# Performance work log

Hardware: AMD Instinct MI355X
Metric: run time of the kernel (lower is better)

## Reference

```python
import jax, jax.numpy as jnp
import numpy as np
from jax import lax

EPS = 1e-5
DN = ('NCHW', 'OIHW', 'NCHW')


def setup_inputs() -> dict:
    key = jax.random.key(0)
    ks = jax.random.split(key, 16)
    B = 8192
    # uniform(0,1): every pixel nonzero => all voxels active => sparse conv == dense conv
    x = jax.random.uniform(ks[0], (B, 1, 28, 28), dtype=jnp.float32)

    def conv_params(kw, kb, c_in, c_out, k):
        scale = 1.0 / np.sqrt(c_in * k * k)
        w = jax.random.normal(kw, (c_out, c_in, k, k), dtype=jnp.float32) * scale
        b = jax.random.normal(kb, (c_out,), dtype=jnp.float32) * scale
        return w, b

    w0, b0 = conv_params(ks[1], ks[2], 1, 32, 3)
    w1, b1 = conv_params(ks[3], ks[4], 32, 64, 2)
    w2, b2 = conv_params(ks[5], ks[6], 64, 128, 2)
    # BatchNorm affine params (init: gamma=1, beta=0)
    g0, be0 = jnp.ones((32,), jnp.float32), jnp.zeros((32,), jnp.float32)
    g1, be1 = jnp.ones((64,), jnp.float32), jnp.zeros((64,), jnp.float32)
    g2, be2 = jnp.ones((128,), jnp.float32), jnp.zeros((128,), jnp.float32)
    w_fc = jax.random.normal(ks[7], (10, 128), dtype=jnp.float32) * (1.0 / np.sqrt(128))
    b_fc = jax.random.normal(ks[8], (10,), dtype=jnp.float32) * (1.0 / np.sqrt(128))
    return dict(x=x, w0=w0, b0=b0, g0=g0, be0=be0,
                w1=w1, b1=b1, g1=g1, be1=be1,
                w2=w2, b2=b2, g2=g2, be2=be2,
                w_fc=w_fc, b_fc=b_fc)


def _conv_bn_relu(x, w, b, g, be, stride, padding):
    # sparse conv on fully-active grid == dense conv
    y = lax.conv_general_dilated(x, w, (stride, stride), padding,
                                 dimension_numbers=DN)
    y = y + b[None, :, None, None]
    # BatchNorm1d over (N_active, C) == stats over batch+spatial (biased var)
    mean = jnp.mean(y, axis=(0, 2, 3))
    var = jnp.var(y, axis=(0, 2, 3))
    y = (y - mean[None, :, None, None]) * lax.rsqrt(var + EPS)[None, :, None, None]
    y = y * g[None, :, None, None] + be[None, :, None, None]
    return jax.nn.relu(y)


def reference(x, w0, b0, g0, be0, w1, b1, g1, be1, w2, b2, g2, be2, w_fc, b_fc):
    h = _conv_bn_relu(x, w0, b0, g0, be0, 1, 'SAME')    # (B,32,28,28)
    h = _conv_bn_relu(h, w1, b1, g1, be1, 2, 'VALID')   # (B,64,14,14)
    h = _conv_bn_relu(h, w2, b2, g2, be2, 2, 'VALID')   # (B,128,7,7)
    pooled = jnp.mean(h, axis=(2, 3))                    # AdaptiveAvgPool2d(1)+Flatten
    return pooled @ w_fc.T + b_fc                        # (B, n_classes)
```

## Files before the change

### kernel.cpp

```cpp
#include <hip/hip_runtime.h>
#include <hip/hip_bf16.h>

typedef __bf16 bf16x8 __attribute__((ext_vector_type(8)));
typedef float  f32x4  __attribute__((ext_vector_type(4)));

#define BSZ 8192

__global__ void k_prep(const float* __restrict__ w1, const float* __restrict__ w2,
                       __bf16* __restrict__ w1b, __bf16* __restrict__ w2b) {
    int t = blockIdx.x * blockDim.x + threadIdx.x;
    if (t < 8192) {
        int oc = t >> 7, k = t & 127, c = k & 31, d = k >> 5;
        w1b[t] = (__bf16)w1[oc * 128 + c * 4 + d];
    }
    if (t < 32768) {
        int oc = t >> 8, k = t & 255, c = k & 63, d = k >> 6;
        w2b[t] = (__bf16)w2[oc * 256 + c * 4 + d];
    }
}

__global__ __launch_bounds__(256) void k_stats0(const float* __restrict__ x,
                                                float* __restrict__ part0) {
    __shared__ float sred[4 * 54];
    const int tid = threadIdx.x;
    float a[54];
#pragma unroll
    for (int i = 0; i < 54; i++) a[i] = 0.f;
    const int total = BSZ * 784;
    for (int p = blockIdx.x * 256 + tid; p < total; p += gridDim.x * 256) {
        int b = p / 784, pix = p - b * 784;
        int y = pix / 28, xx = pix - y * 28;
        const float* xb = x + (long)b * 784;
        float nv[9];
#pragma unroll
        for (int dy = 0; dy < 3; dy++) {
            int yy = y + dy - 1;
#pragma unroll
            for (int dx = 0; dx < 3; dx++) {
                int x2 = xx + dx - 1;
                nv[dy * 3 + dx] = (yy >= 0 && yy < 28 && x2 >= 0 && x2 < 28) ? xb[yy * 28 + x2] : 0.f;
            }
        }
        int idx = 0;
#pragma unroll
        for (int t = 0; t < 9; t++) {
            float vt = nv[t];
            a[45 + t] += vt;
#pragma unroll
            for (int u = t; u < 9; u++) { a[idx] += vt * nv[u]; idx++; }
        }
    }
#pragma unroll
    for (int i = 0; i < 54; i++) {
        float v = a[i];
        v += __shfl_xor(v, 1);  v += __shfl_xor(v, 2);  v += __shfl_xor(v, 4);
        v += __shfl_xor(v, 8);  v += __shfl_xor(v, 16); v += __shfl_xor(v, 32);
        a[i] = v;
    }
    const int l = tid & 63, w = tid >> 6;
    if (l == 0) {
#pragma unroll
        for (int i = 0; i < 54; i++) sred[w * 54 + i] = a[i];
    }
    __syncthreads();
    if (tid < 54)
        part0[blockIdx.x * 64 + tid] = sred[tid] + sred[54 + tid] + sred[108 + tid] + sred[162 + tid];
}

__global__ void k_fin0(const float* __restrict__ part0, const float* __restrict__ w0,
                       const float* __restrict__ g0, const float* __restrict__ be0,
                       float* __restrict__ abc0) {
    __shared__ float red[4 * 54];
    int t = threadIdx.x, c = t & 63, g = t >> 6;
    if (c < 54) {
        float acc = 0.f;
        for (int i = g; i < 1024; i += 4) acc += part0[i * 64 + c];
        red[g * 54 + c] = acc;
    }
    __syncthreads();
    if (t < 54) red[t] = red[t] + red[54 + t] + red[108 + t] + red[162 + t];
    __syncthreads();
    if (t < 32) {
        float wv[9];
#pragma unroll
        for (int tap = 0; tap < 9; tap++) wv[tap] = w0[t * 9 + tap];
        float sum = 0.f, sq = 0.f;
        int idx = 0;
#pragma unroll
        for (int ta = 0; ta < 9; ta++) {
            sum = fmaf(wv[ta], red[45 + ta], sum);
#pragma unroll
            for (int u = ta; u < 9; u++) {
                float coef = (u == ta) ? 1.f : 2.f;
                sq = fmaf(coef * wv[ta] * wv[u], red[idx], sq);
                idx++;
            }
        }
        float cnt = (float)BSZ * 784.f;
        float mean = sum / cnt;
        float var = sq / cnt - mean * mean;
        float A = g0[t] * rsqrtf(var + 1e-5f);
#pragma unroll
        for (int tap = 0; tap < 9; tap++)
            abc0[(t >> 3) * 72 + tap * 8 + (t & 7)] = A * wv[tap];
        abc0[288 + t] = be0[t] - mean * A;
    }
}

__global__ __launch_bounds__(256) void k_conv01(const float* __restrict__ x,
                                                const float* __restrict__ abc0,
                                                const __bf16* __restrict__ w1b,
                                                __bf16* __restrict__ h1,
                                                float* __restrict__ part1) {
    __shared__ float xs[30 * 30];
    __shared__ __attribute__((aligned(16))) __bf16 sAt[2][16 * 136];
    const int b = blockIdx.x, tid = threadIdx.x;
    if (tid < 116) {
        int idx;
        if (tid < 30)      idx = tid;
        else if (tid < 60) idx = 29 * 30 + (tid - 30);
        else if (tid < 88) idx = (tid - 60 + 1) * 30;
        else               idx = (tid - 88 + 1) * 30 + 29;
        xs[idx] = 0.f;
    }
    for (int j = tid; j < 784; j += 256) {
        int yy = j / 28, xx2 = j - yy * 28;
        xs[(yy + 1) * 30 + xx2 + 1] = x[(long)b * 784 + j];
    }
    const int pgu = __builtin_amdgcn_readfirstlane(tid >> 6);
    const float* wfp = abc0 + pgu * 72;
    float wf[72];
#pragma unroll
    for (int i = 0; i < 72; i++) wf[i] = wfp[i];
    float c0r[8];
#pragma unroll
    for (int j = 0; j < 8; j++) c0r[j] = abc0[288 + pgu * 8 + j];

    const int pi = tid & 15, pd = (tid >> 4) & 3;
    const int w = tid >> 6, l = tid & 63, q = l >> 4, n = l & 15;
    const int oc = w * 16 + n;
    bf16x8 fbv[4];
#pragma unroll
    for (int kc = 0; kc < 4; kc++)
        fbv[kc] = *(const bf16x8*)&w1b[oc * 128 + kc * 32 + q * 8];
    float ssum = 0.f, ssq = 0.f;
    __bf16* hb = h1 + (long)b * 12544 + (q * 4) * 64 + oc;
    __syncthreads();

    for (int mt = 0; mt < 13; mt++) {
        __bf16* dst = &sAt[mt & 1][pi * 136 + pd * 32 + pgu * 8];
        int m = mt * 16 + pi;
        bf16x8 pk;
        if (m < 196) {
            int my = m / 14, mx = m - my * 14;
            int y0 = my * 2 + (pd >> 1), x0 = mx * 2 + (pd & 1);
            float nv[9];
#pragma unroll
            for (int dy = 0; dy < 3; dy++)
#pragma unroll
                for (int dx = 0; dx < 3; dx++)
                    nv[dy * 3 + dx] = xs[(y0 + dy) * 30 + x0 + dx];
            float a[8];
#pragma unroll
            for (int j = 0; j < 8; j++) a[j] = c0r[j];
#pragma unroll
            for (int t = 0; t < 9; t++) {
                float nvt = nv[t];
#pragma unroll
                for (int j = 0; j < 8; j++) a[j] = fmaf(nvt, wf[t * 8 + j], a[j]);
            }
#pragma unroll
            for (int j = 0; j < 8; j++) pk[j] = (__bf16)fmaxf(a[j], 0.f);
        } else {
#pragma unroll
            for (int j = 0; j < 8; j++) pk[j] = (__bf16)0.0f;
        }
        *(bf16x8*)dst = pk;
        __syncthreads();
        const __bf16* sa = &sAt[mt & 1][n * 136 + q * 8];
        f32x4 acc = {0.f, 0.f, 0.f, 0.f};
#pragma unroll
        for (int kc = 0; kc < 4; kc++) {
            bf16x8 fav = *(const bf16x8*)&sa[kc * 32];
            acc = __builtin_amdgcn_mfma_f32_16x16x32_bf16(fav, fbv[kc], acc, 0, 0, 0);
        }
        bool valid = (mt < 12) | (q == 0);
        __bf16* hp = hb + mt * 16 * 64;
#pragma unroll
        for (int r = 0; r < 4; r++) {
            __bf16 hv = (__bf16)acc[r];
            if (valid) hp[r * 64] = hv;
            float fv = (float)hv;
            ssum += fv; ssq += fv * fv;
        }
    }
    ssum += __shfl_xor(ssum, 16); ssum += __shfl_xor(ssum, 32);
    ssq  += __shfl_xor(ssq, 16);  ssq  += __shfl_xor(ssq, 32);
    if (l < 16) {
        part1[(long)oc * BSZ + b] = ssum;
        part1[(long)(64 + oc) * BSZ + b] = ssq;
    }
}

__global__ __launch_bounds__(256) void k_redfin(const float* __restrict__ part,
                                                const float* __restrict__ g,
                                                const float* __restrict__ be,
                                                float* __restrict__ abc,
                                                int C, float cnt) {
    __shared__ float s1[256], s2[256];
    const int c = blockIdx.x, tid = threadIdx.x;
    float a = 0.f, bq = 0.f;
    const float* p1 = part + (long)c * BSZ;
    const float* p2 = part + (long)(C + c) * BSZ;
    for (int i = tid; i < BSZ; i += 256) { a += p1[i]; bq += p2[i]; }
    s1[tid] = a; s2[tid] = bq;
    __syncthreads();
    for (int s = 128; s > 0; s >>= 1) {
        if (tid < s) { s1[tid] += s1[tid + s]; s2[tid] += s2[tid + s]; }
        __syncthreads();
    }
    if (tid == 0) {
        float mean = s1[0] / cnt;
        float var = s2[0] / cnt - mean * mean;
        float A = g[c] * rsqrtf(var + 1e-5f);
        abc[c] = A;
        abc[C + c] = be[c] - mean * A;
    }
}

__global__ __launch_bounds__(256) void k_conv2s(__bf16* __restrict__ h1,
                                                const __bf16* __restrict__ w2b,
                                                const float* __restrict__ abc1,
                                                float* __restrict__ part2) {
    __shared__ __attribute__((aligned(16))) __bf16 sAt[2][16 * 264];
    __shared__ float sbn1[128];
    const int b = blockIdx.x, tid = threadIdx.x;
    if (tid < 128) sbn1[tid] = abc1[tid];
    const __bf16* src = h1 + (long)b * 12544;
    const int w = tid >> 6, l = tid & 63, q = l >> 4, n = l & 15;
    bf16x8 fbv[2][8];
#pragma unroll
    for (int ntl = 0; ntl < 2; ntl++) {
        int oc = (2 * w + ntl) * 16 + n;
#pragma unroll
        for (int kc = 0; kc < 8; kc++)
            fbv[ntl][kc] = *(const bf16x8*)&w2b[oc * 256 + kc * 32 + q * 8];
    }
    float ssum[2] = {0.f, 0.f}, ssq[2] = {0.f, 0.f};
    __bf16* zb = h1 + (long)b * 12544 + (q * 4) * 128 + (2 * w) * 16 + n;
    __syncthreads();

    for (int mt = 0; mt < 4; mt++) {
#pragma unroll
        for (int it = 0; it < 2; it++) {
            int idx = it * 256 + tid;
            int rl = idx >> 5, o = (idx & 31) * 8;
            int r = mt * 16 + rl;
            bf16x8 wv;
            if (r < 49) {
                int d = o >> 6, c = o & 63;
                int py = r / 7, px = r - py * 7;
                int msrc = (2 * py + (d >> 1)) * 14 + 2 * px + (d & 1);
                bf16x8 v = *(const bf16x8*)&src[msrc * 64 + c];
#pragma unroll
                for (int j = 0; j < 8; j++) {
                    float f = fmaxf((float)v[j] * sbn1[c + j] + sbn1[64 + c + j], 0.f);
                    wv[j] = (__bf16)f;
                }
            } else {
#pragma unroll
                for (int j = 0; j < 8; j++) wv[j] = (__bf16)0.0f;
            }
            *(bf16x8*)&sAt[mt & 1][rl * 264 + o] = wv;
        }
        __syncthreads();
        bf16x8 fav[8];
#pragma unroll
        for (int kc = 0; kc < 8; kc++)
            fav[kc] = *(const bf16x8*)&sAt[mt & 1][n * 264 + kc * 32 + q * 8];
#pragma unroll
        for (int ntl = 0; ntl < 2; ntl++) {
            f32x4 acc = {0.f, 0.f, 0.f, 0.f};
#pragma unroll
            for (int kc = 0; kc < 8; kc++)
                acc = __builtin_amdgcn_mfma_f32_16x16x32_bf16(fav[kc], fbv[ntl][kc], acc, 0, 0, 0);
            __bf16* zp = zb + mt * 16 * 128 + ntl * 16;
#pragma unroll
            for (int rr = 0; rr < 4; rr++) {
                __bf16 hv = (__bf16)acc[rr];
                int m = mt * 16 + q * 4 + rr;
                if (m < 49) zp[rr * 128] = hv;
                float fv = (float)hv;
                ssum[ntl] += fv; ssq[ntl] += fv * fv;
            }
        }
    }
#pragma unroll
    for (int ntl = 0; ntl < 2; ntl++) {
        ssum[ntl] += __shfl_xor(ssum[ntl], 16); ssum[ntl] += __shfl_xor(ssum[ntl], 32);
        ssq[ntl]  += __shfl_xor(ssq[ntl], 16);  ssq[ntl]  += __shfl_xor(ssq[ntl], 32);
    }
    if (l < 16) {
#pragma unroll
        for (int ntl = 0; ntl < 2; ntl++) {
            int oc = (2 * w + ntl) * 16 + l;
            part2[(long)oc * BSZ + b] = ssum[ntl];
            part2[(long)(128 + oc) * BSZ + b] = ssq[ntl];
        }
    }
}

__global__ __launch_bounds__(256) void k_final(const __bf16* __restrict__ z2,
                                               const float* __restrict__ abc2,
                                               const float* __restrict__ wfc,
                                               const float* __restrict__ bfc,
                                               float* __restrict__ out) {
    __shared__ float sbn2[256];
    __shared__ float pp[16 * 128];
    __shared__ float pooled[128];
    __shared__ float fcred[80];
    const int b = blockIdx.x, tid = threadIdx.x;
    sbn2[tid] = abc2[tid];
    __syncthreads();
    const int g = tid & 15, c0 = g * 8, rg = tid >> 4;
    const __bf16* src = z2 + (long)b * 12544;
    float acc[8];
#pragma unroll
    for (int q = 0; q < 8; q++) acc[q] = 0.f;
    for (int rr = rg; rr < 49; rr += 16) {
        bf16x8 v = *(const bf16x8*)&src[rr * 128 + c0];
#pragma unroll
        for (int q = 0; q < 8; q++) {
            float f = fmaxf((float)v[q] * sbn2[c0 + q] + sbn2[128 + c0 + q], 0.f);
            acc[q] += f;
        }
    }
    *(f32x4*)&pp[rg * 128 + c0]     = *(f32x4*)&acc[0];
    *(f32x4*)&pp[rg * 128 + c0 + 4] = *(f32x4*)&acc[4];
    __syncthreads();
    if (tid < 128) {
        float s = 0.f;
#pragma unroll
        for (int r = 0; r < 16; r++) s += pp[r * 128 + tid];
        pooled[tid] = s * (1.f / 49.f);
    }
    __syncthreads();
    if (tid < 80) {
        int o = tid >> 3, s = tid & 7;
        float a = 0.f;
#pragma unroll
        for (int j = 0; j < 16; j++) a = fmaf(pooled[s * 16 + j], wfc[o * 128 + s * 16 + j], a);
        fcred[tid] = a;
    }
    __syncthreads();
    if (tid < 10) {
        float a = bfc[tid];
#pragma unroll
        for (int s = 0; s < 8; s++) a += fcred[tid * 8 + s];
        out[(long)b * 10 + tid] = a;
    }
}

extern "C" void kernel_launch(void* const* d_in, const int* in_sizes, int n_in,
                              void* d_out, int out_size, void* d_ws, size_t ws_size,
                              hipStream_t stream) {
    const float* x   = (const float*)d_in[0];
    const float* w0  = (const float*)d_in[1];
    const float* g0  = (const float*)d_in[3];
    const float* be0 = (const float*)d_in[4];
    const float* w1  = (const float*)d_in[5];
    const float* g1  = (const float*)d_in[7];
    const float* be1 = (const float*)d_in[8];
    const float* w2  = (const float*)d_in[9];
    const float* g2  = (const float*)d_in[11];
    const float* be2 = (const float*)d_in[12];
    const float* wfc = (const float*)d_in[13];
    const float* bfc = (const float*)d_in[14];
    float* out = (float*)d_out;

    float* ws    = (float*)d_ws;
    float* part0 = ws;
    float* abc0  = part0 + 1024 * 64;
    float* part1 = abc0 + 320;
    float* abc1  = part1 + 128 * BSZ;
    float* part2 = abc1 + 128;
    float* abc2  = part2 + 256 * BSZ;
    __bf16* w1b  = (__bf16*)(abc2 + 256);
    __bf16* w2b  = w1b + 8192;
    __bf16* h1   = w2b + 32768;

    k_prep<<<dim3(128), dim3(256), 0, stream>>>(w1, w2, w1b, w2b);
    k_stats0<<<dim3(1024), dim3(256), 0, stream>>>(x, part0);
    k_fin0<<<dim3(1), dim3(256), 0, stream>>>(part0, w0, g0, be0, abc0);
    k_conv01<<<dim3(BSZ), dim3(256), 0, stream>>>(x, abc0, w1b, h1, part1);
    k_redfin<<<dim3(64), dim3(256), 0, stream>>>(part1, g1, be1, abc1, 64, (float)(BSZ * 196));
    k_conv2s<<<dim3(BSZ), dim3(256), 0, stream>>>(h1, w2b, abc1, part2);
    k_redfin<<<dim3(128), dim3(256), 0, stream>>>(part2, g2, be2, abc2, 128, (float)(BSZ * 49));
    k_final<<<dim3(BSZ), dim3(256), 0, stream>>>(h1, abc2, wfc, bfc, out);
}
```

Before: 431.2 us.

## Process four images per block and fold weight prep into stats kernel

The conv01, conv2s and final kernels now loop over four images per block, with grids a quarter the size. Per-block setup such as loading weight fragments, BN coefficients and the zeroed halo is paid once per four images instead of once per image. The weight bf16 conversion moves into k_stats0, which removes one kernel launch. conv2s now stages its output tile in shared memory so global stores are row-contiguous, at the cost of an extra barrier per tile. With fewer blocks there is less parallelism to hide latency, and each block has a longer serial chain.

```diff
diff --git a/kernel.cpp b/kernel.cpp
--- a/kernel.cpp
+++ b/kernel.cpp
@@ -6,23 +6,25 @@
 
 #define BSZ 8192
 
-__global__ void k_prep(const float* __restrict__ w1, const float* __restrict__ w2,
-                       __bf16* __restrict__ w1b, __bf16* __restrict__ w2b) {
-    int t = blockIdx.x * blockDim.x + threadIdx.x;
-    if (t < 8192) {
-        int oc = t >> 7, k = t & 127, c = k & 31, d = k >> 5;
-        w1b[t] = (__bf16)w1[oc * 128 + c * 4 + d];
-    }
-    if (t < 32768) {
-        int oc = t >> 8, k = t & 255, c = k & 63, d = k >> 6;
-        w2b[t] = (__bf16)w2[oc * 256 + c * 4 + d];
-    }
-}
-
 __global__ __launch_bounds__(256) void k_stats0(const float* __restrict__ x,
-                                                float* __restrict__ part0) {
+                                                float* __restrict__ part0,
+                                                const float* __restrict__ w1,
+                                                const float* __restrict__ w2,
+                                                __bf16* __restrict__ w1b,
+                                                __bf16* __restrict__ w2b) {
     __shared__ float sred[4 * 54];
     const int tid = threadIdx.x;
+    {
+        int t = blockIdx.x * 256 + tid;
+        if (t < 8192) {
+            int oc = t >> 7, k = t & 127, c = k & 31, d = k >> 5;
+            w1b[t] = (__bf16)w1[oc * 128 + c * 4 + d];
+        }
+        if (t < 32768) {
+            int oc = t >> 8, k = t & 255, c = k & 63, d = k >> 6;
+            w2b[t] = (__bf16)w2[oc * 256 + c * 4 + d];
+        }
+    }
     float a[54];
 #pragma unroll
     for (int i = 0; i < 54; i++) a[i] = 0.f;
@@ -43,11 +45,11 @@
         }
         int idx = 0;
 #pragma unroll
-        for (int t = 0; t < 9; t++) {
-            float vt = nv[t];
-            a[45 + t] += vt;
-#pragma unroll
-            for (int u = t; u < 9; u++) { a[idx] += vt * nv[u]; idx++; }
+        for (int t2 = 0; t2 < 9; t2++) {
+            float vt = nv[t2];
+            a[45 + t2] += vt;
+#pragma unroll
+            for (int u = t2; u < 9; u++) { a[idx] += vt * nv[u]; idx++; }
         }
     }
 #pragma unroll
@@ -114,7 +116,7 @@
                                                 float* __restrict__ part1) {
     __shared__ float xs[30 * 30];
     __shared__ __attribute__((aligned(16))) __bf16 sAt[2][16 * 136];
-    const int b = blockIdx.x, tid = threadIdx.x;
+    const int tid = threadIdx.x;
     if (tid < 116) {
         int idx;
         if (tid < 30)      idx = tid;
@@ -123,10 +125,6 @@
         else               idx = (tid - 88 + 1) * 30 + 29;
         xs[idx] = 0.f;
     }
-    for (int j = tid; j < 784; j += 256) {
-        int yy = j / 28, xx2 = j - yy * 28;
-        xs[(yy + 1) * 30 + xx2 + 1] = x[(long)b * 784 + j];
-    }
     const int pgu = __builtin_amdgcn_readfirstlane(tid >> 6);
     const float* wfp = abc0 + pgu * 72;
     float wf[72];
@@ -143,62 +141,69 @@
 #pragma unroll
     for (int kc = 0; kc < 4; kc++)
         fbv[kc] = *(const bf16x8*)&w1b[oc * 128 + kc * 32 + q * 8];
-    float ssum = 0.f, ssq = 0.f;
-    __bf16* hb = h1 + (long)b * 12544 + (q * 4) * 64 + oc;
-    __syncthreads();
-
-    for (int mt = 0; mt < 13; mt++) {
-        __bf16* dst = &sAt[mt & 1][pi * 136 + pd * 32 + pgu * 8];
-        int m = mt * 16 + pi;
-        bf16x8 pk;
-        if (m < 196) {
-            int my = m / 14, mx = m - my * 14;
-            int y0 = my * 2 + (pd >> 1), x0 = mx * 2 + (pd & 1);
-            float nv[9];
-#pragma unroll
-            for (int dy = 0; dy < 3; dy++)
-#pragma unroll
-                for (int dx = 0; dx < 3; dx++)
-                    nv[dy * 3 + dx] = xs[(y0 + dy) * 30 + x0 + dx];
-            float a[8];
-#pragma unroll
-            for (int j = 0; j < 8; j++) a[j] = c0r[j];
-#pragma unroll
-            for (int t = 0; t < 9; t++) {
-                float nvt = nv[t];
-#pragma unroll
-                for (int j = 0; j < 8; j++) a[j] = fmaf(nvt, wf[t * 8 + j], a[j]);
-            }
-#pragma unroll
-            for (int j = 0; j < 8; j++) pk[j] = (__bf16)fmaxf(a[j], 0.f);
-        } else {
-#pragma unroll
-            for (int j = 0; j < 8; j++) pk[j] = (__bf16)0.0f;
-        }
-        *(bf16x8*)dst = pk;
+
+    for (int img = 0; img < 4; img++) {
+        const int b = blockIdx.x * 4 + img;
+        for (int j = tid; j < 784; j += 256) {
+            int yy = j / 28, xx2 = j - yy * 28;
+            xs[(yy + 1) * 30 + xx2 + 1] = x[(long)b * 784 + j];
+        }
         __syncthreads();
-        const __bf16* sa = &sAt[mt & 1][n * 136 + q * 8];
-        f32x4 acc = {0.f, 0.f, 0.f, 0.f};
-#pragma unroll
-        for (int kc = 0; kc < 4; kc++) {
-            bf16x8 fav = *(const bf16x8*)&sa[kc * 32];
-            acc = __builtin_amdgcn_mfma_f32_16x16x32_bf16(fav, fbv[kc], acc, 0, 0, 0);
-        }
-        bool valid = (mt < 12) | (q == 0);
-        __bf16* hp = hb + mt * 16 * 64;
-#pragma unroll
-        for (int r = 0; r < 4; r++) {
-            __bf16 hv = (__bf16)acc[r];
-            if (valid) hp[r * 64] = hv;
-            float fv = (float)hv;
-            ssum += fv; ssq += fv * fv;
-        }
-    }
-    ssum += __shfl_xor(ssum, 16); ssum += __shfl_xor(ssum, 32);
-    ssq  += __shfl_xor(ssq, 16);  ssq  += __shfl_xor(ssq, 32);
-    if (l < 16) {
-        part1[(long)oc * BSZ + b] = ssum;
-        part1[(long)(64 + oc) * BSZ + b] = ssq;
+        float ssum = 0.f, ssq = 0.f;
+        __bf16* hb = h1 + (long)b * 12544 + (q * 4) * 64 + oc;
+        for (int mt = 0; mt < 13; mt++) {
+            __bf16* dst = &sAt[mt & 1][pi * 136 + pd * 32 + pgu * 8];
+            int m = mt * 16 + pi;
+            bf16x8 pk;
+            if (m < 196) {
+                int my = m / 14, mx = m - my * 14;
+                int y0 = my * 2 + (pd >> 1), x0 = mx * 2 + (pd & 1);
+                float nv[9];
+#pragma unroll
+                for (int dy = 0; dy < 3; dy++)
+#pragma unroll
+                    for (int dx = 0; dx < 3; dx++)
+                        nv[dy * 3 + dx] = xs[(y0 + dy) * 30 + x0 + dx];
+                float a[8];
+#pragma unroll
+                for (int j = 0; j < 8; j++) a[j] = c0r[j];
+#pragma unroll
+                for (int t = 0; t < 9; t++) {
+                    float nvt = nv[t];
+#pragma unroll
+                    for (int j = 0; j < 8; j++) a[j] = fmaf(nvt, wf[t * 8 + j], a[j]);
+                }
+#pragma unroll
+                for (int j = 0; j < 8; j++) pk[j] = (__bf16)fmaxf(a[j], 0.f);
+            } else {
+#pragma unroll
+                for (int j = 0; j < 8; j++) pk[j] = (__bf16)0.0f;
+            }
+            *(bf16x8*)dst = pk;
+            __syncthreads();
+            const __bf16* sa = &sAt[mt & 1][n * 136 + q * 8];
+            f32x4 acc = {0.f, 0.f, 0.f, 0.f};
+#pragma unroll
+            for (int kc = 0; kc < 4; kc++) {
+                bf16x8 fav = *(const bf16x8*)&sa[kc * 32];
+                acc = __builtin_amdgcn_mfma_f32_16x16x32_bf16(fav, fbv[kc], acc, 0, 0, 0);
+            }
+            bool valid = (mt < 12) | (q == 0);
+            __bf16* hp = hb + mt * 16 * 64;
+#pragma unroll
+            for (int r = 0; r < 4; r++) {
+                __bf16 hv = (__bf16)acc[r];
+                if (valid) hp[r * 64] = hv;
+                float fv = (float)hv;
+                ssum += fv; ssq += fv * fv;
+            }
+        }
+        ssum += __shfl_xor(ssum, 16); ssum += __shfl_xor(ssum, 32);
+        ssq  += __shfl_xor(ssq, 16);  ssq  += __shfl_xor(ssq, 32);
+        if (l < 16) {
+            part1[(long)oc * BSZ + b] = ssum;
+            part1[(long)(64 + oc) * BSZ + b] = ssq;
+        }
     }
 }
 
@@ -233,10 +238,10 @@
                                                 const float* __restrict__ abc1,
                                                 float* __restrict__ part2) {
     __shared__ __attribute__((aligned(16))) __bf16 sAt[2][16 * 264];
+    __shared__ __attribute__((aligned(16))) __bf16 zt[16 * 136];
     __shared__ float sbn1[128];
-    const int b = blockIdx.x, tid = threadIdx.x;
+    const int tid = threadIdx.x;
     if (tid < 128) sbn1[tid] = abc1[tid];
-    const __bf16* src = h1 + (long)b * 12544;
     const int w = tid >> 6, l = tid & 63, q = l >> 4, n = l & 15;
     bf16x8 fbv[2][8];
 #pragma unroll
@@ -246,66 +251,76 @@
         for (int kc = 0; kc < 8; kc++)
             fbv[ntl][kc] = *(const bf16x8*)&w2b[oc * 256 + kc * 32 + q * 8];
     }
-    float ssum[2] = {0.f, 0.f}, ssq[2] = {0.f, 0.f};
-    __bf16* zb = h1 + (long)b * 12544 + (q * 4) * 128 + (2 * w) * 16 + n;
-    __syncthreads();
-
-    for (int mt = 0; mt < 4; mt++) {
-#pragma unroll
-        for (int it = 0; it < 2; it++) {
-            int idx = it * 256 + tid;
-            int rl = idx >> 5, o = (idx & 31) * 8;
-            int r = mt * 16 + rl;
-            bf16x8 wv;
-            if (r < 49) {
-                int d = o >> 6, c = o & 63;
-                int py = r / 7, px = r - py * 7;
-                int msrc = (2 * py + (d >> 1)) * 14 + 2 * px + (d & 1);
-                bf16x8 v = *(const bf16x8*)&src[msrc * 64 + c];
-#pragma unroll
-                for (int j = 0; j < 8; j++) {
-                    float f = fmaxf((float)v[j] * sbn1[c + j] + sbn1[64 + c + j], 0.f);
-                    wv[j] = (__bf16)f;
+    __syncthreads();
+
+    for (int img = 0; img < 4; img++) {
+        const int b = blockIdx.x * 4 + img;
+        __bf16* src = h1 + (long)b * 12544;
+        float ssum[2] = {0.f, 0.f}, ssq[2] = {0.f, 0.f};
+        for (int mt = 0; mt < 4; mt++) {
+#pragma unroll
+            for (int it = 0; it < 2; it++) {
+                int idx = it * 256 + tid;
+                int rl = idx >> 5, o = (idx & 31) * 8;
+                int r = mt * 16 + rl;
+                bf16x8 wv;
+                if (r < 49) {
+                    int d = o >> 6, c = o & 63;
+                    int py = r / 7, px = r - py * 7;
+                    int msrc = (2 * py + (d >> 1)) * 14 + 2 * px + (d & 1);
+                    bf16x8 v = *(const bf16x8*)&src[msrc * 64 + c];
+#pragma unroll
+                    for (int j = 0; j < 8; j++) {
+                        float f = fmaxf((float)v[j] * sbn1[c + j] + sbn1[64 + c + j], 0.f);
+                        wv[j] = (__bf16)f;
+                    }
+                } else {
+#pragma unroll
+                    for (int j = 0; j < 8; j++) wv[j] = (__bf16)0.0f;
                 }
-            } else {
-#pragma unroll
-                for (int j = 0; j < 8; j++) wv[j] = (__bf16)0.0f;
-            }
-            *(bf16x8*)&sAt[mt & 1][rl * 264 + o] = wv;
-        }
-        __syncthreads();
-        bf16x8 fav[8];
-#pragma unroll
-        for (int kc = 0; kc < 8; kc++)
-            fav[kc] = *(const bf16x8*)&sAt[mt & 1][n * 264 + kc * 32 + q * 8];
+                *(bf16x8*)&sAt[mt & 1][rl * 264 + o] = wv;
+            }
+            __syncthreads();
+            bf16x8 fav[8];
+#pragma unroll
+            for (int kc = 0; kc < 8; kc++)
+                fav[kc] = *(const bf16x8*)&sAt[mt & 1][n * 264 + kc * 32 + q * 8];
+#pragma unroll
+            for (int ntl = 0; ntl < 2; ntl++) {
+                f32x4 acc = {0.f, 0.f, 0.f, 0.f};
+#pragma unroll
+                for (int kc = 0; kc < 8; kc++)
+                    acc = __builtin_amdgcn_mfma_f32_16x16x32_bf16(fav[kc], fbv[ntl][kc], acc, 0, 0, 0);
+#pragma unroll
+                for (int rr = 0; rr < 4; rr++) {
+                    __bf16 hv = (__bf16)acc[rr];
+                    zt[(q * 4 + rr) * 136 + (2 * w + ntl) * 16 + n] = hv;
+                    float fv = (float)hv;
+                    ssum[ntl] += fv; ssq[ntl] += fv * fv;
+                }
+            }
+            __syncthreads();
+            {
+                int row = tid >> 4, o = (tid & 15) * 8;
+                int m = mt * 16 + row;
+                if (m < 49) {
+                    bf16x8 zv = *(const bf16x8*)&zt[row * 136 + o];
+                    *(bf16x8*)&src[m * 128 + o] = zv;
+                }
+            }
+        }
 #pragma unroll
         for (int ntl = 0; ntl < 2; ntl++) {
-            f32x4 acc = {0.f, 0.f, 0.f, 0.f};
-#pragma unroll
-            for (int kc = 0; kc < 8; kc++)
-                acc = __builtin_amdgcn_mfma_f32_16x16x32_bf16(fav[kc], fbv[ntl][kc], acc, 0, 0, 0);
-            __bf16* zp = zb + mt * 16 * 128 + ntl * 16;
-#pragma unroll
-            for (int rr = 0; rr < 4; rr++) {
-                __bf16 hv = (__bf16)acc[rr];
-                int m = mt * 16 + q * 4 + rr;
-                if (m < 49) zp[rr * 128] = hv;
-                float fv = (float)hv;
-                ssum[ntl] += fv; ssq[ntl] += fv * fv;
-            }
-        }
-    }
-#pragma unroll
-    for (int ntl = 0; ntl < 2; ntl++) {
-        ssum[ntl] += __shfl_xor(ssum[ntl], 16); ssum[ntl] += __shfl_xor(ssum[ntl], 32);
-        ssq[ntl]  += __shfl_xor(ssq[ntl], 16);  ssq[ntl]  += __shfl_xor(ssq[ntl], 32);
-    }
-    if (l < 16) {
-#pragma unroll
-        for (int ntl = 0; ntl < 2; ntl++) {
-            int oc = (2 * w + ntl) * 16 + l;
-            part2[(long)oc * BSZ + b] = ssum[ntl];
-            part2[(long)(128 + oc) * BSZ + b] = ssq[ntl];
+            ssum[ntl] += __shfl_xor(ssum[ntl], 16); ssum[ntl] += __shfl_xor(ssum[ntl], 32);
+            ssq[ntl]  += __shfl_xor(ssq[ntl], 16);  ssq[ntl]  += __shfl_xor(ssq[ntl], 32);
+        }
+        if (l < 16) {
+#pragma unroll
+            for (int ntl = 0; ntl < 2; ntl++) {
+                int oc = (2 * w + ntl) * 16 + l;
+                part2[(long)oc * BSZ + b] = ssum[ntl];
+                part2[(long)(128 + oc) * BSZ + b] = ssq[ntl];
+            }
         }
     }
 }
@@ -319,45 +334,48 @@
     __shared__ float pp[16 * 128];
     __shared__ float pooled[128];
     __shared__ float fcred[80];
-    const int b = blockIdx.x, tid = threadIdx.x;
+    const int tid = threadIdx.x;
     sbn2[tid] = abc2[tid];
     __syncthreads();
     const int g = tid & 15, c0 = g * 8, rg = tid >> 4;
-    const __bf16* src = z2 + (long)b * 12544;
-    float acc[8];
-#pragma unroll
-    for (int q = 0; q < 8; q++) acc[q] = 0.f;
-    for (int rr = rg; rr < 49; rr += 16) {
-        bf16x8 v = *(const bf16x8*)&src[rr * 128 + c0];
-#pragma unroll
-        for (int q = 0; q < 8; q++) {
-            float f = fmaxf((float)v[q] * sbn2[c0 + q] + sbn2[128 + c0 + q], 0.f);
-            acc[q] += f;
-        }
-    }
-    *(f32x4*)&pp[rg * 128 + c0]     = *(f32x4*)&acc[0];
-    *(f32x4*)&pp[rg * 128 + c0 + 4] = *(f32x4*)&acc[4];
-    __syncthreads();
-    if (tid < 128) {
-        float s = 0.f;
-#pragma unroll
-        for (int r = 0; r < 16; r++) s += pp[r * 128 + tid];
-        pooled[tid] = s * (1.f / 49.f);
-    }
-    __syncthreads();
-    if (tid < 80) {
-        int o = tid >> 3, s = tid & 7;
-        float a = 0.f;
-#pragma unroll
-        for (int j = 0; j < 16; j++) a = fmaf(pooled[s * 16 + j], wfc[o * 128 + s * 16 + j], a);
-        fcred[tid] = a;
-    }
-    __syncthreads();
-    if (tid < 10) {
-        float a = bfc[tid];
-#pragma unroll
-        for (int s = 0; s < 8; s++) a += fcred[tid * 8 + s];
-        out[(long)b * 10 + tid] = a;
+    for (int img = 0; img < 4; img++) {
+        const int b = blockIdx.x * 4 + img;
+        const __bf16* src = z2 + (long)b * 12544;
+        float acc[8];
+#pragma unroll
+        for (int q = 0; q < 8; q++) acc[q] = 0.f;
+        for (int rr = rg; rr < 49; rr += 16) {
+            bf16x8 v = *(const bf16x8*)&src[rr * 128 + c0];
+#pragma unroll
+            for (int q = 0; q < 8; q++) {
+                float f = fmaxf((float)v[q] * sbn2[c0 + q] + sbn2[128 + c0 + q], 0.f);
+                acc[q] += f;
+            }
+        }
+        *(f32x4*)&pp[rg * 128 + c0]     = *(f32x4*)&acc[0];
+        *(f32x4*)&pp[rg * 128 + c0 + 4] = *(f32x4*)&acc[4];
+        __syncthreads();
+        if (tid < 128) {
+            float s = 0.f;
+#pragma unroll
+            for (int r = 0; r < 16; r++) s += pp[r * 128 + tid];
+            pooled[tid] = s * (1.f / 49.f);
+        }
+        __syncthreads();
+        if (tid < 80) {
+            int o = tid >> 3, s = tid & 7;
+            float a = 0.f;
+#pragma unroll
+            for (int j = 0; j < 16; j++) a = fmaf(pooled[s * 16 + j], wfc[o * 128 + s * 16 + j], a);
+            fcred[tid] = a;
+        }
+        __syncthreads();
+        if (tid < 10) {
+            float a = bfc[tid];
+#pragma unroll
+            for (int s = 0; s < 8; s++) a += fcred[tid * 8 + s];
+            out[(long)b * 10 + tid] = a;
+        }
     }
 }
 
@@ -389,12 +407,11 @@
     __bf16* w2b  = w1b + 8192;
     __bf16* h1   = w2b + 32768;
 
-    k_prep<<<dim3(128), dim3(256), 0, stream>>>(w1, w2, w1b, w2b);
-    k_stats0<<<dim3(1024), dim3(256), 0, stream>>>(x, part0);
+    k_stats0<<<dim3(1024), dim3(256), 0, stream>>>(x, part0, w1, w2, w1b, w2b);
     k_fin0<<<dim3(1), dim3(256), 0, stream>>>(part0, w0, g0, be0, abc0);
-    k_conv01<<<dim3(BSZ), dim3(256), 0, stream>>>(x, abc0, w1b, h1, part1);
+    k_conv01<<<dim3(BSZ / 4), dim3(256), 0, stream>>>(x, abc0, w1b, h1, part1);
     k_redfin<<<dim3(64), dim3(256), 0, stream>>>(part1, g1, be1, abc1, 64, (float)(BSZ * 196));
-    k_conv2s<<<dim3(BSZ), dim3(256), 0, stream>>>(h1, w2b, abc1, part2);
+    k_conv2s<<<dim3(BSZ / 4), dim3(256), 0, stream>>>(h1, w2b, abc1, part2);
     k_redfin<<<dim3(128), dim3(256), 0, stream>>>(part2, g2, be2, abc2, 128, (float)(BSZ * 49));
-    k_final<<<dim3(BSZ), dim3(256), 0, stream>>>(h1, abc2, wfc, bfc, out);
-}
+    k_final<<<dim3(BSZ / 4), dim3(256), 0, stream>>>(h1, abc2, wfc, bfc, out);
+}
```

After: 410.1 us. 1.05x faster.
